# Optimization experiments

Measured on AMD Instinct MI355X. Metric: run time of the kernel, lower is better.

Reference implementation:

```python
import jax, jax.numpy as jnp
import numpy as np

N = 100000      # total nodes (flattened batch)
E = 640000      # total edges
D = 128         # in_channels
SIM_THR = 0.2   # pt_dict['sim_pt']
DEG_THR = 3.0   # pt_dict['degree_pt']
PT_THRESHOLD = 0.1  # edge-pruning cosine threshold
EPS = 1e-8      # F.cosine_similarity eps


def _glorot(key, shape):
    a = np.sqrt(6.0 / (shape[-2] + shape[-1]))
    return jax.random.uniform(key, shape, jnp.float32, -a, a)


def setup_inputs() -> dict:
    key = jax.random.key(0)
    k1, k2, k3, k4, k5 = jax.random.split(key, 5)
    x = jax.random.normal(k1, (N, D), jnp.float32)
    edge_index = jax.random.randint(k2, (2, E), 0, N, dtype=jnp.int32)
    p_sim = _glorot(k3, (1, D))
    p_deg = _glorot(k4, (1, D))
    p_other = _glorot(k5, (1, D))
    return {"x": x, "edge_index": edge_index, "p_sim": p_sim, "p_deg": p_deg, "p_other": p_other}


def reference(x, edge_index, p_sim, p_deg, p_other):
    n = x.shape[0]
    row, col = edge_index[0], edge_index[1]

    # --- sim_pt: per-edge cosine of raw features, scatter-add to dst, degree-normalize ---
    x_norm = x / jnp.sqrt(jnp.sum(x * x, axis=1, keepdims=True))          # [N, D]
    e = jnp.sum(x_norm[row] * x_norm[col], axis=1)                         # [E]
    c = jax.ops.segment_sum(e, col, num_segments=n)                        # [N]
    deg = jax.ops.segment_sum(jnp.ones_like(e), col, num_segments=n)       # [N]
    # torch: c/deg -> nan for deg==0, nan <= thr is False; +inf gives the same mask, safely.
    csim = jnp.where(deg > 0, c / jnp.maximum(deg, 1.0), jnp.inf)
    mask_sim = csim <= SIM_THR                                             # [N]

    # --- degree_pt ---
    mask_deg = deg <= DEG_THR                                              # [N]

    # --- other_pt == 'all': nodes that got no prompt so far ---
    mask_other = ~(mask_sim | mask_deg)                                    # [N]

    # g_mutiftpt_record: [N, 3, D], slot filled with its prompt row where mask else 0
    masks = jnp.stack([mask_sim, mask_deg, mask_other], axis=1)            # [N, 3]
    prompts = jnp.concatenate([p_sim, p_deg, p_other], axis=0)             # [3, D]
    record = masks[:, :, None].astype(x.dtype) * prompts[None, :, :]       # [N, 3, D]

    # use_attention=False branch: mean over non-padding (all-nonzero) slots
    wo_pad = jnp.all(record != 0, axis=-1)                                 # [N, 3]
    plen = jnp.sum(wo_pad, axis=1, keepdims=True).astype(x.dtype)          # [N, 1]
    final = jnp.where(plen > 0, record.sum(axis=1) / jnp.maximum(plen, 1.0), 0.0)  # [N, D]

    x_new = x + final                                                      # add_pt

    # edge pruning by cosine similarity of prompted features (F.cosine_similarity, eps=1e-8)
    nrm = jnp.sqrt(jnp.sum(x_new * x_new, axis=1))                         # [N]
    na = jnp.maximum(nrm[row], EPS)
    nb = jnp.maximum(nrm[col], EPS)
    cos = jnp.sum(x_new[row] * x_new[col], axis=1) / (na * nb)             # [E]
    keep_edges = cos >= PT_THRESHOLD                                       # [E] bool mask (edge list is static-shape; mask instead of compaction)
    return x_new, keep_edges
```

## Files before the change

### kernel.cpp

```cpp
#include <hip/hip_runtime.h>
#include <hip/hip_bf16.h>
#include <math.h>

#define D_DIM 128
#define SIM_THR 0.2f
#define DEG_THR 3.0f
#define PT_THR 0.1
#define EPS_CS 1e-8
#define MARGIN 4e-3f
#define PK 4294967296.0

typedef unsigned short u16;

#define WS_NEED 8960064

__device__ __forceinline__ float bf2f(u16 u) {
    return __uint_as_float(((unsigned)u) << 16);
}

__global__ void prompt_pre_kernel(const float* __restrict__ ps,
                                  const float* __restrict__ pd,
                                  const float* __restrict__ po,
                                  int* __restrict__ flags,
                                  float* __restrict__ G) {
    int t = threadIdx.x;
    float s0 = ps[t], s1 = ps[t + 64];
    float d0 = pd[t], d1 = pd[t + 64];
    float o0 = po[t], o1 = po[t + 64];
    float ss = s0 * s0 + s1 * s1;
    float sd = s0 * d0 + s1 * d1;
    float so = s0 * o0 + s1 * o1;
    float dd = d0 * d0 + d1 * d1;
    float dO = d0 * o0 + d1 * o1;
    float oo = o0 * o0 + o1 * o1;
    for (int m = 32; m; m >>= 1) {
        ss += __shfl_xor(ss, m);
        sd += __shfl_xor(sd, m);
        so += __shfl_xor(so, m);
        dd += __shfl_xor(dd, m);
        dO += __shfl_xor(dO, m);
        oo += __shfl_xor(oo, m);
    }
    unsigned long long zs = __ballot(s0 == 0.0f || s1 == 0.0f);
    unsigned long long zd = __ballot(d0 == 0.0f || d1 == 0.0f);
    unsigned long long zo = __ballot(o0 == 0.0f || o1 == 0.0f);
    if (t == 0) {
        flags[0] = (zs == 0ull);
        flags[1] = (zd == 0ull);
        flags[2] = (zo == 0ull);
        G[0] = ss; G[1] = sd; G[2] = so;
        G[3] = sd; G[4] = dd; G[5] = dO;
        G[6] = so; G[7] = dO; G[8] = oo;
    }
}

__global__ void node_pre_kernel(const float* __restrict__ x,
                                const float* __restrict__ ps,
                                const float* __restrict__ pd,
                                const float* __restrict__ po,
                                u16* __restrict__ xnorm,
                                float* __restrict__ nx,
                                float* __restrict__ rs,
                                float* __restrict__ rd,
                                float* __restrict__ ro, int N) {
    int g = threadIdx.x >> 5;
    int lane = threadIdx.x & 31;
    int n = blockIdx.x * 8 + g;
    if (n >= N) return;
    int off = lane * 4;
    const float4 v = *(const float4*)(x + (size_t)n * D_DIM + off);
    const float4 s = *(const float4*)(ps + off);
    const float4 d = *(const float4*)(pd + off);
    const float4 o = *(const float4*)(po + off);
    float sq = v.x * v.x + v.y * v.y + v.z * v.z + v.w * v.w;
    float drs = v.x * s.x + v.y * s.y + v.z * s.z + v.w * s.w;
    float drd = v.x * d.x + v.y * d.y + v.z * d.z + v.w * d.w;
    float dro = v.x * o.x + v.y * o.y + v.z * o.z + v.w * o.w;
    for (int m = 16; m; m >>= 1) {
        sq += __shfl_xor(sq, m, 32);
        drs += __shfl_xor(drs, m, 32);
        drd += __shfl_xor(drd, m, 32);
        dro += __shfl_xor(dro, m, 32);
    }
    float nrm = sqrtf(sq);
    float inv = 1.0f / nrm;
    __hip_bfloat16 ob[4];
    ob[0] = __float2bfloat16(v.x * inv);
    ob[1] = __float2bfloat16(v.y * inv);
    ob[2] = __float2bfloat16(v.z * inv);
    ob[3] = __float2bfloat16(v.w * inv);
    *(ushort4*)(xnorm + (size_t)n * D_DIM + off) =
        make_ushort4(*(u16*)&ob[0], *(u16*)&ob[1], *(u16*)&ob[2], *(u16*)&ob[3]);
    if (lane == 0) {
        nx[n] = nrm;
        rs[n] = drs;
        rd[n] = drd;
        ro[n] = dro;
    }
}

__global__ void edge_sim_kernel(const u16* __restrict__ xnorm,
                                const int* __restrict__ ei,
                                double* __restrict__ cd,
                                float* __restrict__ e_arr,
                                int E) {
    int lane = threadIdx.x & 31;
    int grp = blockIdx.x * 8 + (threadIdx.x >> 5);
    int base = grp * 4;
    if (base >= E) return;

    int r[4], c4[4];
    #pragma unroll
    for (int k = 0; k < 4; ++k) {
        int e = base + k;
        int src = (e < E) ? e : base;
        r[k] = ei[src];
        c4[k] = ei[E + src];
    }

    ushort4 a[4], b[4];
    #pragma unroll
    for (int k = 0; k < 4; ++k) {
        a[k] = *(const ushort4*)(xnorm + (size_t)r[k] * D_DIM + lane * 4);
        b[k] = *(const ushort4*)(xnorm + (size_t)c4[k] * D_DIM + lane * 4);
    }

    float d[4];
    #pragma unroll
    for (int k = 0; k < 4; ++k) {
        d[k] = bf2f(a[k].x) * bf2f(b[k].x) + bf2f(a[k].y) * bf2f(b[k].y) +
               bf2f(a[k].z) * bf2f(b[k].z) + bf2f(a[k].w) * bf2f(b[k].w);
    }
    for (int m = 16; m; m >>= 1) {
        #pragma unroll
        for (int k = 0; k < 4; ++k) d[k] += __shfl_xor(d[k], m, 32);
    }

    if (lane < 4) {
        int e = base + lane;
        if (e < E) {
            float dv = (lane == 0) ? d[0] : (lane == 1) ? d[1] : (lane == 2) ? d[2] : d[3];
            if (e_arr) e_arr[e] = dv;
            atomicAdd(&cd[c4[lane]], (double)dv + PK);
        }
    }
}

__global__ void node_prompt_kernel(const float* __restrict__ x,
                                   const double* __restrict__ cd,
                                   const float* __restrict__ ps,
                                   const float* __restrict__ pd,
                                   const float* __restrict__ po,
                                   const int* __restrict__ flags,
                                   const float* __restrict__ nx,
                                   const float* __restrict__ rs,
                                   const float* __restrict__ rd,
                                   const float* __restrict__ ro,
                                   float* __restrict__ xn,
                                   double* __restrict__ na,
                                   float* __restrict__ pack, int N) {
    int g = threadIdx.x >> 5;
    int lane = threadIdx.x & 31;
    int n = blockIdx.x * 8 + g;
    if (n >= N) return;
    double v = cd[n];
    double degd = floor(v * (1.0 / PK) + 0.5);
    float dg = (float)degd;
    float cc = (float)(v - degd * PK);
    float csim = (dg > 0.0f) ? (cc / fmaxf(dg, 1.0f)) : INFINITY;
    bool ms = (csim <= SIM_THR);
    bool md = (dg <= DEG_THR);
    bool mo = !(ms || md);
    int plen = (ms && flags[0]) + (md && flags[1]) + (mo && flags[2]);
    float invp = (plen > 0) ? (1.0f / (float)plen) : 0.0f;

    int off = lane * 4;
    const float4 xv = *(const float4*)(x + (size_t)n * D_DIM + off);
    const float4 s  = *(const float4*)(ps + off);
    const float4 dd = *(const float4*)(pd + off);
    const float4 o  = *(const float4*)(po + off);

    float4 f;
    f.x = (ms ? s.x : 0.0f) + (md ? dd.x : 0.0f) + (mo ? o.x : 0.0f);
    f.y = (ms ? s.y : 0.0f) + (md ? dd.y : 0.0f) + (mo ? o.y : 0.0f);
    f.z = (ms ? s.z : 0.0f) + (md ? dd.z : 0.0f) + (mo ? o.z : 0.0f);
    f.w = (ms ? s.w : 0.0f) + (md ? dd.w : 0.0f) + (mo ? o.w : 0.0f);

    float4 r;
    r.x = xv.x + f.x * invp;
    r.y = xv.y + f.y * invp;
    r.z = xv.z + f.z * invp;
    r.w = xv.w + f.w * invp;

    *(float4*)(xn + (size_t)n * D_DIM + off) = r;

    double sq = (double)r.x * r.x + (double)r.y * r.y + (double)r.z * r.z + (double)r.w * r.w;
    for (int m = 16; m; m >>= 1) sq += __shfl_xor(sq, m, 32);
    if (lane == 0) {
        double nrm = sqrt(sq);
        double nad = (nrm > EPS_CS) ? nrm : EPS_CS;
        na[n] = nad;
        if (pack) {
            float as = ms ? invp : 0.0f;
            float ad = md ? invp : 0.0f;
            float ao = mo ? invp : 0.0f;
            float4 w0 = make_float4(rs[n], rd[n], ro[n], nx[n]);
            float4 w1 = make_float4(as, ad, ao, (float)(1.0 / nad));
            *(float4*)(pack + (size_t)n * 8)     = w0;
            *(float4*)(pack + (size_t)n * 8 + 4) = w1;
        }
    }
}

__global__ void edge_prune_fused(const int* __restrict__ ei,
                                 const float* __restrict__ e_arr,
                                 const float* __restrict__ pack,
                                 const float* __restrict__ G,
                                 const float* __restrict__ xn,
                                 const double* __restrict__ na,
                                 float* __restrict__ keep, int E) {
    __shared__ int s_list[256];
    __shared__ int s_cnt;
    int tid = threadIdx.x;
    if (tid == 0) s_cnt = 0;
    __syncthreads();

    int e = blockIdx.x * 256 + tid;
    if (e < E) {
        int i = ei[e], j = ei[E + e];
        const float4 ri = *(const float4*)(pack + (size_t)i * 8);
        const float4 ai = *(const float4*)(pack + (size_t)i * 8 + 4);
        const float4 rj = *(const float4*)(pack + (size_t)j * 8);
        const float4 aj = *(const float4*)(pack + (size_t)j * 8 + 4);
        float ev = e_arr[e];
        float dot = ev * ri.w * rj.w
                  + aj.x * ri.x + aj.y * ri.y + aj.z * ri.z
                  + ai.x * rj.x + ai.y * rj.y + ai.z * rj.z;
        dot += ai.x * (G[0] * aj.x + G[1] * aj.y + G[2] * aj.z)
             + ai.y * (G[3] * aj.x + G[4] * aj.y + G[5] * aj.z)
             + ai.z * (G[6] * aj.x + G[7] * aj.y + G[8] * aj.z);
        float cosv = dot * ai.w * aj.w;
        keep[e] = (cosv >= 0.1f) ? 1.0f : 0.0f;
        if (fabsf(cosv - 0.1f) < MARGIN) {
            int idx = atomicAdd(&s_cnt, 1);
            s_list[idx] = e;
        }
    }
    __syncthreads();

    int cnt = s_cnt;
    int lane = tid & 31;
    int grp = tid >> 5;
    for (int it = grp; it < cnt; it += 8) {
        int ee = s_list[it];
        int row = ei[ee], col = ei[E + ee];
        const float4 a = *(const float4*)(xn + (size_t)row * D_DIM + lane * 4);
        const float4 b = *(const float4*)(xn + (size_t)col * D_DIM + lane * 4);
        double d = (double)a.x * b.x + (double)a.y * b.y +
                   (double)a.z * b.z + (double)a.w * b.w;
        for (int m = 16; m; m >>= 1) d += __shfl_xor(d, m, 32);
        if (lane == 0) {
            double cs = d / (na[row] * na[col]);
            keep[ee] = (cs >= PT_THR) ? 1.0f : 0.0f;
        }
    }
}

__global__ void edge_prune_kernel(const float* __restrict__ xn,
                                  const int* __restrict__ ei,
                                  const double* __restrict__ na,
                                  float* __restrict__ keep, int E) {
    int lane = threadIdx.x & 31;
    int grp = blockIdx.x * 8 + (threadIdx.x >> 5);
    int e0 = grp * 2, e1 = e0 + 1;
    if (e0 >= E) return;
    bool has1 = (e1 < E);
    int row0 = ei[e0], col0 = ei[E + e0];
    int row1 = has1 ? ei[e1] : row0;
    int col1 = has1 ? ei[E + e1] : col0;

    const float4 a0 = *(const float4*)(xn + (size_t)row0 * D_DIM + lane * 4);
    const float4 b0 = *(const float4*)(xn + (size_t)col0 * D_DIM + lane * 4);
    const float4 a1 = *(const float4*)(xn + (size_t)row1 * D_DIM + lane * 4);
    const float4 b1 = *(const float4*)(xn + (size_t)col1 * D_DIM + lane * 4);

    double d0 = (double)a0.x * b0.x + (double)a0.y * b0.y +
                (double)a0.z * b0.z + (double)a0.w * b0.w;
    double d1 = (double)a1.x * b1.x + (double)a1.y * b1.y +
                (double)a1.z * b1.z + (double)a1.w * b1.w;
    for (int m = 16; m; m >>= 1) {
        d0 += __shfl_xor(d0, m, 32);
        d1 += __shfl_xor(d1, m, 32);
    }
    if (lane == 0) {
        double cs = d0 / (na[row0] * na[col0]);
        keep[e0] = (cs >= PT_THR) ? 1.0f : 0.0f;
    } else if (lane == 1 && has1) {
        double cs = d1 / (na[row1] * na[col1]);
        keep[e1] = (cs >= PT_THR) ? 1.0f : 0.0f;
    }
}

extern "C" void kernel_launch(void* const* d_in, const int* in_sizes, int n_in,
                              void* d_out, int out_size, void* d_ws, size_t ws_size,
                              hipStream_t stream) {
    const float* x  = (const float*)d_in[0];
    const int*   ei = (const int*)d_in[1];
    const float* ps = (const float*)d_in[2];
    const float* pd = (const float*)d_in[3];
    const float* po = (const float*)d_in[4];

    const int N = in_sizes[0] / D_DIM;
    const int E = in_sizes[1] / 2;

    float* xn    = (float*)d_out;
    float* keep  = (float*)d_out + (size_t)N * D_DIM;
    u16*   xnorm = (u16*)d_out;

    char* ws = (char*)d_ws;
    const int nodeBlocks = (N + 7) / 8;
    const int simBlocks  = (E + 31) / 32;

    if (ws_size >= (size_t)WS_NEED) {
        double* cd    = (double*)(ws + 0);
        double* na    = (double*)(ws + 800000);
        float* nx     = (float*)(ws + 1600000);
        float* rs     = (float*)(ws + 2000000);
        float* rd     = (float*)(ws + 2400000);
        float* ro     = (float*)(ws + 2800000);
        float* e_arr  = (float*)(ws + 3200000);
        float* pack   = (float*)(ws + 5760000);
        int*   flags  = (int*)(ws + 8960000);
        float* G      = (float*)(ws + 8960016);

        hipMemsetAsync(cd, 0, 800000, stream);

        prompt_pre_kernel<<<1, 64, 0, stream>>>(ps, pd, po, flags, G);
        node_pre_kernel<<<nodeBlocks, 256, 0, stream>>>(x, ps, pd, po, xnorm, nx, rs, rd, ro, N);
        edge_sim_kernel<<<simBlocks, 256, 0, stream>>>(xnorm, ei, cd, e_arr, E);
        node_prompt_kernel<<<nodeBlocks, 256, 0, stream>>>(x, cd, ps, pd, po,
                                                           flags, nx, rs, rd, ro,
                                                           xn, na, pack, N);
        edge_prune_fused<<<(E + 255) / 256, 256, 0, stream>>>(ei, e_arr, pack, G, xn, na, keep, E);
    } else {
        double* cd    = (double*)(ws + 0);
        double* na    = (double*)(ws + 800000);
        int*   flags  = (int*)(ws + 1600000);
        float* G      = (float*)(ws + 1600016);
        float* scratch = (float*)(ws + 1600064);

        hipMemsetAsync(cd, 0, 800000, stream);
        prompt_pre_kernel<<<1, 64, 0, stream>>>(ps, pd, po, flags, G);
        node_pre_kernel<<<nodeBlocks, 256, 0, stream>>>(x, ps, pd, po, xnorm,
                                                        scratch, scratch, scratch, scratch, N);
        edge_sim_kernel<<<simBlocks, 256, 0, stream>>>(xnorm, ei, cd, nullptr, E);
        node_prompt_kernel<<<nodeBlocks, 256, 0, stream>>>(x, cd, ps, pd, po,
                                                           flags, nullptr, nullptr, nullptr, nullptr,
                                                           xn, na, nullptr, N);
        edge_prune_kernel<<<(E + 15) / 16, 256, 0, stream>>>(xn, ei, na, keep, E);
    }
}
```

Before: 107.6 us.

## Partition edge-sim atomics by destination range per XCD and fuse prep kernels

The edge similarity kernel now has each block take a chunk of edges and filter, into shared memory, only those whose destination node falls in the range assigned to that block's XCD (blockIdx mod 8). The aim is to keep the double-precision scatter atomics for a node range inside one XCD's L2. The memset of the accumulator and the prompt precompute kernel are folded into node_pre_kernel, removing two launches. In exchange, every block rereads the column indices for its chunk (8x redundant index reads), compacts the list with a shared atomic counter, and relies on blocks being assigned to XCDs round-robin.

```diff
diff --git a/kernel.cpp b/kernel.cpp
--- a/kernel.cpp
+++ b/kernel.cpp
@@ -9,6 +9,8 @@
 #define EPS_CS 1e-8
 #define MARGIN 4e-3f
 #define PK 4294967296.0
+#define CHUNK 2048
+#define NXCD 8
 
 typedef unsigned short u16;
 
@@ -16,42 +18,6 @@
 
 __device__ __forceinline__ float bf2f(u16 u) {
     return __uint_as_float(((unsigned)u) << 16);
-}
-
-__global__ void prompt_pre_kernel(const float* __restrict__ ps,
-                                  const float* __restrict__ pd,
-                                  const float* __restrict__ po,
-                                  int* __restrict__ flags,
-                                  float* __restrict__ G) {
-    int t = threadIdx.x;
-    float s0 = ps[t], s1 = ps[t + 64];
-    float d0 = pd[t], d1 = pd[t + 64];
-    float o0 = po[t], o1 = po[t + 64];
-    float ss = s0 * s0 + s1 * s1;
-    float sd = s0 * d0 + s1 * d1;
-    float so = s0 * o0 + s1 * o1;
-    float dd = d0 * d0 + d1 * d1;
-    float dO = d0 * o0 + d1 * o1;
-    float oo = o0 * o0 + o1 * o1;
-    for (int m = 32; m; m >>= 1) {
-        ss += __shfl_xor(ss, m);
-        sd += __shfl_xor(sd, m);
-        so += __shfl_xor(so, m);
-        dd += __shfl_xor(dd, m);
-        dO += __shfl_xor(dO, m);
-        oo += __shfl_xor(oo, m);
-    }
-    unsigned long long zs = __ballot(s0 == 0.0f || s1 == 0.0f);
-    unsigned long long zd = __ballot(d0 == 0.0f || d1 == 0.0f);
-    unsigned long long zo = __ballot(o0 == 0.0f || o1 == 0.0f);
-    if (t == 0) {
-        flags[0] = (zs == 0ull);
-        flags[1] = (zd == 0ull);
-        flags[2] = (zo == 0ull);
-        G[0] = ss; G[1] = sd; G[2] = so;
-        G[3] = sd; G[4] = dd; G[5] = dO;
-        G[6] = so; G[7] = dO; G[8] = oo;
-    }
 }
 
 __global__ void node_pre_kernel(const float* __restrict__ x,
@@ -62,86 +28,146 @@
                                 float* __restrict__ nx,
                                 float* __restrict__ rs,
                                 float* __restrict__ rd,
-                                float* __restrict__ ro, int N) {
+                                float* __restrict__ ro,
+                                double* __restrict__ cd,
+                                int* __restrict__ flags,
+                                float* __restrict__ G, int N) {
     int g = threadIdx.x >> 5;
     int lane = threadIdx.x & 31;
     int n = blockIdx.x * 8 + g;
-    if (n >= N) return;
-    int off = lane * 4;
-    const float4 v = *(const float4*)(x + (size_t)n * D_DIM + off);
-    const float4 s = *(const float4*)(ps + off);
-    const float4 d = *(const float4*)(pd + off);
-    const float4 o = *(const float4*)(po + off);
-    float sq = v.x * v.x + v.y * v.y + v.z * v.z + v.w * v.w;
-    float drs = v.x * s.x + v.y * s.y + v.z * s.z + v.w * s.w;
-    float drd = v.x * d.x + v.y * d.y + v.z * d.z + v.w * d.w;
-    float dro = v.x * o.x + v.y * o.y + v.z * o.z + v.w * o.w;
-    for (int m = 16; m; m >>= 1) {
-        sq += __shfl_xor(sq, m, 32);
-        drs += __shfl_xor(drs, m, 32);
-        drd += __shfl_xor(drd, m, 32);
-        dro += __shfl_xor(dro, m, 32);
-    }
-    float nrm = sqrtf(sq);
-    float inv = 1.0f / nrm;
-    __hip_bfloat16 ob[4];
-    ob[0] = __float2bfloat16(v.x * inv);
-    ob[1] = __float2bfloat16(v.y * inv);
-    ob[2] = __float2bfloat16(v.z * inv);
-    ob[3] = __float2bfloat16(v.w * inv);
-    *(ushort4*)(xnorm + (size_t)n * D_DIM + off) =
-        make_ushort4(*(u16*)&ob[0], *(u16*)&ob[1], *(u16*)&ob[2], *(u16*)&ob[3]);
-    if (lane == 0) {
-        nx[n] = nrm;
-        rs[n] = drs;
-        rd[n] = drd;
-        ro[n] = dro;
-    }
-}
-
-__global__ void edge_sim_kernel(const u16* __restrict__ xnorm,
-                                const int* __restrict__ ei,
-                                double* __restrict__ cd,
-                                float* __restrict__ e_arr,
-                                int E) {
-    int lane = threadIdx.x & 31;
-    int grp = blockIdx.x * 8 + (threadIdx.x >> 5);
-    int base = grp * 4;
-    if (base >= E) return;
-
-    int r[4], c4[4];
-    #pragma unroll
-    for (int k = 0; k < 4; ++k) {
-        int e = base + k;
-        int src = (e < E) ? e : base;
-        r[k] = ei[src];
-        c4[k] = ei[E + src];
-    }
-
-    ushort4 a[4], b[4];
-    #pragma unroll
-    for (int k = 0; k < 4; ++k) {
-        a[k] = *(const ushort4*)(xnorm + (size_t)r[k] * D_DIM + lane * 4);
-        b[k] = *(const ushort4*)(xnorm + (size_t)c4[k] * D_DIM + lane * 4);
-    }
-
-    float d[4];
-    #pragma unroll
-    for (int k = 0; k < 4; ++k) {
-        d[k] = bf2f(a[k].x) * bf2f(b[k].x) + bf2f(a[k].y) * bf2f(b[k].y) +
-               bf2f(a[k].z) * bf2f(b[k].z) + bf2f(a[k].w) * bf2f(b[k].w);
-    }
-    for (int m = 16; m; m >>= 1) {
+    if (n < N) {
+        int off = lane * 4;
+        const float4 v = *(const float4*)(x + (size_t)n * D_DIM + off);
+        const float4 s = *(const float4*)(ps + off);
+        const float4 d = *(const float4*)(pd + off);
+        const float4 o = *(const float4*)(po + off);
+        float sq = v.x * v.x + v.y * v.y + v.z * v.z + v.w * v.w;
+        float drs = v.x * s.x + v.y * s.y + v.z * s.z + v.w * s.w;
+        float drd = v.x * d.x + v.y * d.y + v.z * d.z + v.w * d.w;
+        float dro = v.x * o.x + v.y * o.y + v.z * o.z + v.w * o.w;
+        for (int m = 16; m; m >>= 1) {
+            sq += __shfl_xor(sq, m, 32);
+            drs += __shfl_xor(drs, m, 32);
+            drd += __shfl_xor(drd, m, 32);
+            dro += __shfl_xor(dro, m, 32);
+        }
+        float nrm = sqrtf(sq);
+        float inv = 1.0f / nrm;
+        __hip_bfloat16 ob[4];
+        ob[0] = __float2bfloat16(v.x * inv);
+        ob[1] = __float2bfloat16(v.y * inv);
+        ob[2] = __float2bfloat16(v.z * inv);
+        ob[3] = __float2bfloat16(v.w * inv);
+        *(ushort4*)(xnorm + (size_t)n * D_DIM + off) =
+            make_ushort4(*(u16*)&ob[0], *(u16*)&ob[1], *(u16*)&ob[2], *(u16*)&ob[3]);
+        if (lane == 0) {
+            nx[n] = nrm;
+            rs[n] = drs;
+            rd[n] = drd;
+            ro[n] = dro;
+            cd[n] = 0.0;
+        }
+    }
+    if (blockIdx.x == 0 && threadIdx.x < 64) {
+        int t = threadIdx.x;
+        float s0 = ps[t], s1 = ps[t + 64];
+        float d0 = pd[t], d1 = pd[t + 64];
+        float o0 = po[t], o1 = po[t + 64];
+        float ss = s0 * s0 + s1 * s1;
+        float sd = s0 * d0 + s1 * d1;
+        float so = s0 * o0 + s1 * o1;
+        float dd = d0 * d0 + d1 * d1;
+        float dO = d0 * o0 + d1 * o1;
+        float oo = o0 * o0 + o1 * o1;
+        for (int m = 32; m; m >>= 1) {
+            ss += __shfl_xor(ss, m);
+            sd += __shfl_xor(sd, m);
+            so += __shfl_xor(so, m);
+            dd += __shfl_xor(dd, m);
+            dO += __shfl_xor(dO, m);
+            oo += __shfl_xor(oo, m);
+        }
+        unsigned long long zs = __ballot(s0 == 0.0f || s1 == 0.0f);
+        unsigned long long zd = __ballot(d0 == 0.0f || d1 == 0.0f);
+        unsigned long long zo = __ballot(o0 == 0.0f || o1 == 0.0f);
+        if (t == 0) {
+            flags[0] = (zs == 0ull);
+            flags[1] = (zd == 0ull);
+            flags[2] = (zo == 0ull);
+            G[0] = ss; G[1] = sd; G[2] = so;
+            G[3] = sd; G[4] = dd; G[5] = dO;
+            G[6] = so; G[7] = dO; G[8] = oo;
+        }
+    }
+}
+
+__global__ void edge_sim_part(const u16* __restrict__ xnorm,
+                              const int* __restrict__ ei,
+                              double* __restrict__ cd,
+                              float* __restrict__ e_arr,
+                              int E, int N) {
+    __shared__ int s_list[CHUNK];
+    __shared__ int s_cnt;
+    int tid = threadIdx.x;
+    if (tid == 0) s_cnt = 0;
+    __syncthreads();
+
+    int xcd = blockIdx.x & (NXCD - 1);
+    int base = (blockIdx.x >> 3) * CHUNK;
+    int range = (N + NXCD - 1) / NXCD;
+    int lo = xcd * range;
+    int hi = min(N, lo + range);
+
+    for (int i = tid; i < CHUNK; i += 256) {
+        int e = base + i;
+        if (e < E) {
+            int col = ei[E + e];
+            if (col >= lo && col < hi) {
+                int idx = atomicAdd(&s_cnt, 1);
+                s_list[idx] = e;
+            }
+        }
+    }
+    __syncthreads();
+
+    int cnt = s_cnt;
+    int lane = tid & 31;
+    int grp = tid >> 5;
+    for (int b = grp * 4; b < cnt; b += 32) {
+        int r[4], c4[4];
         #pragma unroll
-        for (int k = 0; k < 4; ++k) d[k] += __shfl_xor(d[k], m, 32);
-    }
-
-    if (lane < 4) {
-        int e = base + lane;
-        if (e < E) {
-            float dv = (lane == 0) ? d[0] : (lane == 1) ? d[1] : (lane == 2) ? d[2] : d[3];
-            if (e_arr) e_arr[e] = dv;
-            atomicAdd(&cd[c4[lane]], (double)dv + PK);
+        for (int k = 0; k < 4; ++k) {
+            int p = b + k;
+            int src = s_list[(p < cnt) ? p : b];
+            r[k] = ei[src];
+            c4[k] = ei[E + src];
+        }
+        ushort4 a[4], bb[4];
+        #pragma unroll
+        for (int k = 0; k < 4; ++k) {
+            a[k]  = *(const ushort4*)(xnorm + (size_t)r[k] * D_DIM + lane * 4);
+            bb[k] = *(const ushort4*)(xnorm + (size_t)c4[k] * D_DIM + lane * 4);
+        }
+        float d[4];
+        #pragma unroll
+        for (int k = 0; k < 4; ++k) {
+            d[k] = bf2f(a[k].x) * bf2f(bb[k].x) + bf2f(a[k].y) * bf2f(bb[k].y) +
+                   bf2f(a[k].z) * bf2f(bb[k].z) + bf2f(a[k].w) * bf2f(bb[k].w);
+        }
+        for (int m = 16; m; m >>= 1) {
+            #pragma unroll
+            for (int k = 0; k < 4; ++k) d[k] += __shfl_xor(d[k], m, 32);
+        }
+        if (lane < 4) {
+            int p = b + lane;
+            if (p < cnt) {
+                int e = s_list[p];
+                int col = ei[E + e];
+                float dv = (lane == 0) ? d[0] : (lane == 1) ? d[1]
+                         : (lane == 2) ? d[2] : d[3];
+                if (e_arr) e_arr[e] = dv;
+                atomicAdd(&cd[col], (double)dv + PK);
+            }
         }
     }
 }
@@ -319,7 +345,7 @@
 
     char* ws = (char*)d_ws;
     const int nodeBlocks = (N + 7) / 8;
-    const int simBlocks  = (E + 31) / 32;
+    const int simBlocks  = ((E + CHUNK - 1) / CHUNK) * NXCD;
 
     if (ws_size >= (size_t)WS_NEED) {
         double* cd    = (double*)(ws + 0);
@@ -333,11 +359,9 @@
         int*   flags  = (int*)(ws + 8960000);
         float* G      = (float*)(ws + 8960016);
 
-        hipMemsetAsync(cd, 0, 800000, stream);
-
-        prompt_pre_kernel<<<1, 64, 0, stream>>>(ps, pd, po, flags, G);
-        node_pre_kernel<<<nodeBlocks, 256, 0, stream>>>(x, ps, pd, po, xnorm, nx, rs, rd, ro, N);
-        edge_sim_kernel<<<simBlocks, 256, 0, stream>>>(xnorm, ei, cd, e_arr, E);
+        node_pre_kernel<<<nodeBlocks, 256, 0, stream>>>(x, ps, pd, po, xnorm,
+                                                        nx, rs, rd, ro, cd, flags, G, N);
+        edge_sim_part<<<simBlocks, 256, 0, stream>>>(xnorm, ei, cd, e_arr, E, N);
         node_prompt_kernel<<<nodeBlocks, 256, 0, stream>>>(x, cd, ps, pd, po,
                                                            flags, nx, rs, rd, ro,
                                                            xn, na, pack, N);
@@ -349,11 +373,10 @@
         float* G      = (float*)(ws + 1600016);
         float* scratch = (float*)(ws + 1600064);
 
-        hipMemsetAsync(cd, 0, 800000, stream);
-        prompt_pre_kernel<<<1, 64, 0, stream>>>(ps, pd, po, flags, G);
         node_pre_kernel<<<nodeBlocks, 256, 0, stream>>>(x, ps, pd, po, xnorm,
-                                                        scratch, scratch, scratch, scratch, N);
-        edge_sim_kernel<<<simBlocks, 256, 0, stream>>>(xnorm, ei, cd, nullptr, E);
+                                                        scratch, scratch, scratch, scratch,
+                                                        cd, flags, G, N);
+        edge_sim_part<<<simBlocks, 256, 0, stream>>>(xnorm, ei, cd, nullptr, E, N);
         node_prompt_kernel<<<nodeBlocks, 256, 0, stream>>>(x, cd, ps, pd, po,
                                                            flags, nullptr, nullptr, nullptr, nullptr,
                                                            xn, na, nullptr, N);
```

New measurement: 115.8 us. 1.08x slower.

## Fold memset and prompt precompute into node_pre; widen edge_sim to 8 edges per group

Applied to the files above, without the earlier changes.

Removes the separate hipMemsetAsync of the per-node accumulator and the one-block prompt_pre launch. The zeroing moves into node_pre_kernel, written per node, and block 0 computes the prompt Gram matrix and flags. The edge similarity kernel now processes 8 edges per 32-lane group instead of 4, halving the grid and doubling gathers in flight per thread. The cost is more registers per thread in edge_sim, and the early return in node_pre is replaced by a guarded branch so block 0 can still run the prompt code.

```diff
diff --git a/kernel.cpp b/kernel.cpp
--- a/kernel.cpp
+++ b/kernel.cpp
@@ -16,42 +16,6 @@
 
 __device__ __forceinline__ float bf2f(u16 u) {
     return __uint_as_float(((unsigned)u) << 16);
-}
-
-__global__ void prompt_pre_kernel(const float* __restrict__ ps,
-                                  const float* __restrict__ pd,
-                                  const float* __restrict__ po,
-                                  int* __restrict__ flags,
-                                  float* __restrict__ G) {
-    int t = threadIdx.x;
-    float s0 = ps[t], s1 = ps[t + 64];
-    float d0 = pd[t], d1 = pd[t + 64];
-    float o0 = po[t], o1 = po[t + 64];
-    float ss = s0 * s0 + s1 * s1;
-    float sd = s0 * d0 + s1 * d1;
-    float so = s0 * o0 + s1 * o1;
-    float dd = d0 * d0 + d1 * d1;
-    float dO = d0 * o0 + d1 * o1;
-    float oo = o0 * o0 + o1 * o1;
-    for (int m = 32; m; m >>= 1) {
-        ss += __shfl_xor(ss, m);
-        sd += __shfl_xor(sd, m);
-        so += __shfl_xor(so, m);
-        dd += __shfl_xor(dd, m);
-        dO += __shfl_xor(dO, m);
-        oo += __shfl_xor(oo, m);
-    }
-    unsigned long long zs = __ballot(s0 == 0.0f || s1 == 0.0f);
-    unsigned long long zd = __ballot(d0 == 0.0f || d1 == 0.0f);
-    unsigned long long zo = __ballot(o0 == 0.0f || o1 == 0.0f);
-    if (t == 0) {
-        flags[0] = (zs == 0ull);
-        flags[1] = (zd == 0ull);
-        flags[2] = (zo == 0ull);
-        G[0] = ss; G[1] = sd; G[2] = so;
-        G[3] = sd; G[4] = dd; G[5] = dO;
-        G[6] = so; G[7] = dO; G[8] = oo;
-    }
 }
 
 __global__ void node_pre_kernel(const float* __restrict__ x,
@@ -62,40 +26,76 @@
                                 float* __restrict__ nx,
                                 float* __restrict__ rs,
                                 float* __restrict__ rd,
-                                float* __restrict__ ro, int N) {
+                                float* __restrict__ ro,
+                                double* __restrict__ cd,
+                                int* __restrict__ flags,
+                                float* __restrict__ G, int N) {
     int g = threadIdx.x >> 5;
     int lane = threadIdx.x & 31;
     int n = blockIdx.x * 8 + g;
-    if (n >= N) return;
-    int off = lane * 4;
-    const float4 v = *(const float4*)(x + (size_t)n * D_DIM + off);
-    const float4 s = *(const float4*)(ps + off);
-    const float4 d = *(const float4*)(pd + off);
-    const float4 o = *(const float4*)(po + off);
-    float sq = v.x * v.x + v.y * v.y + v.z * v.z + v.w * v.w;
-    float drs = v.x * s.x + v.y * s.y + v.z * s.z + v.w * s.w;
-    float drd = v.x * d.x + v.y * d.y + v.z * d.z + v.w * d.w;
-    float dro = v.x * o.x + v.y * o.y + v.z * o.z + v.w * o.w;
-    for (int m = 16; m; m >>= 1) {
-        sq += __shfl_xor(sq, m, 32);
-        drs += __shfl_xor(drs, m, 32);
-        drd += __shfl_xor(drd, m, 32);
-        dro += __shfl_xor(dro, m, 32);
-    }
-    float nrm = sqrtf(sq);
-    float inv = 1.0f / nrm;
-    __hip_bfloat16 ob[4];
-    ob[0] = __float2bfloat16(v.x * inv);
-    ob[1] = __float2bfloat16(v.y * inv);
-    ob[2] = __float2bfloat16(v.z * inv);
-    ob[3] = __float2bfloat16(v.w * inv);
-    *(ushort4*)(xnorm + (size_t)n * D_DIM + off) =
-        make_ushort4(*(u16*)&ob[0], *(u16*)&ob[1], *(u16*)&ob[2], *(u16*)&ob[3]);
-    if (lane == 0) {
-        nx[n] = nrm;
-        rs[n] = drs;
-        rd[n] = drd;
-        ro[n] = dro;
+    if (n < N) {
+        int off = lane * 4;
+        const float4 v = *(const float4*)(x + (size_t)n * D_DIM + off);
+        const float4 s = *(const float4*)(ps + off);
+        const float4 d = *(const float4*)(pd + off);
+        const float4 o = *(const float4*)(po + off);
+        float sq = v.x * v.x + v.y * v.y + v.z * v.z + v.w * v.w;
+        float drs = v.x * s.x + v.y * s.y + v.z * s.z + v.w * s.w;
+        float drd = v.x * d.x + v.y * d.y + v.z * d.z + v.w * d.w;
+        float dro = v.x * o.x + v.y * o.y + v.z * o.z + v.w * o.w;
+        for (int m = 16; m; m >>= 1) {
+            sq += __shfl_xor(sq, m, 32);
+            drs += __shfl_xor(drs, m, 32);
+            drd += __shfl_xor(drd, m, 32);
+            dro += __shfl_xor(dro, m, 32);
+        }
+        float nrm = sqrtf(sq);
+        float inv = 1.0f / nrm;
+        __hip_bfloat16 ob[4];
+        ob[0] = __float2bfloat16(v.x * inv);
+        ob[1] = __float2bfloat16(v.y * inv);
+        ob[2] = __float2bfloat16(v.z * inv);
+        ob[3] = __float2bfloat16(v.w * inv);
+        *(ushort4*)(xnorm + (size_t)n * D_DIM + off) =
+            make_ushort4(*(u16*)&ob[0], *(u16*)&ob[1], *(u16*)&ob[2], *(u16*)&ob[3]);
+        if (lane == 0) {
+            nx[n] = nrm;
+            rs[n] = drs;
+            rd[n] = drd;
+            ro[n] = dro;
+            cd[n] = 0.0;
+        }
+    }
+    if (blockIdx.x == 0 && threadIdx.x < 64) {
+        int t = threadIdx.x;
+        float s0 = ps[t], s1 = ps[t + 64];
+        float d0 = pd[t], d1 = pd[t + 64];
+        float o0 = po[t], o1 = po[t + 64];
+        float ss = s0 * s0 + s1 * s1;
+        float sd = s0 * d0 + s1 * d1;
+        float so = s0 * o0 + s1 * o1;
+        float dd = d0 * d0 + d1 * d1;
+        float dO = d0 * o0 + d1 * o1;
+        float oo = o0 * o0 + o1 * o1;
+        for (int m = 32; m; m >>= 1) {
+            ss += __shfl_xor(ss, m);
+            sd += __shfl_xor(sd, m);
+            so += __shfl_xor(so, m);
+            dd += __shfl_xor(dd, m);
+            dO += __shfl_xor(dO, m);
+            oo += __shfl_xor(oo, m);
+        }
+        unsigned long long zs = __ballot(s0 == 0.0f || s1 == 0.0f);
+        unsigned long long zd = __ballot(d0 == 0.0f || d1 == 0.0f);
+        unsigned long long zo = __ballot(o0 == 0.0f || o1 == 0.0f);
+        if (t == 0) {
+            flags[0] = (zs == 0ull);
+            flags[1] = (zd == 0ull);
+            flags[2] = (zo == 0ull);
+            G[0] = ss; G[1] = sd; G[2] = so;
+            G[3] = sd; G[4] = dd; G[5] = dO;
+            G[6] = so; G[7] = dO; G[8] = oo;
+        }
     }
 }
 
@@ -106,42 +106,49 @@
                                 int E) {
     int lane = threadIdx.x & 31;
     int grp = blockIdx.x * 8 + (threadIdx.x >> 5);
-    int base = grp * 4;
+    int base = grp * 8;
     if (base >= E) return;
 
-    int r[4], c4[4];
+    int r[8], c8[8];
     #pragma unroll
-    for (int k = 0; k < 4; ++k) {
+    for (int k = 0; k < 8; ++k) {
         int e = base + k;
         int src = (e < E) ? e : base;
         r[k] = ei[src];
-        c4[k] = ei[E + src];
-    }
-
-    ushort4 a[4], b[4];
+        c8[k] = ei[E + src];
+    }
+
+    ushort4 a[8], b[8];
     #pragma unroll
-    for (int k = 0; k < 4; ++k) {
+    for (int k = 0; k < 8; ++k) {
         a[k] = *(const ushort4*)(xnorm + (size_t)r[k] * D_DIM + lane * 4);
-        b[k] = *(const ushort4*)(xnorm + (size_t)c4[k] * D_DIM + lane * 4);
-    }
-
-    float d[4];
+        b[k] = *(const ushort4*)(xnorm + (size_t)c8[k] * D_DIM + lane * 4);
+    }
+
+    float d[8];
     #pragma unroll
-    for (int k = 0; k < 4; ++k) {
+    for (int k = 0; k < 8; ++k) {
         d[k] = bf2f(a[k].x) * bf2f(b[k].x) + bf2f(a[k].y) * bf2f(b[k].y) +
                bf2f(a[k].z) * bf2f(b[k].z) + bf2f(a[k].w) * bf2f(b[k].w);
     }
     for (int m = 16; m; m >>= 1) {
         #pragma unroll
-        for (int k = 0; k < 4; ++k) d[k] += __shfl_xor(d[k], m, 32);
-    }
-
-    if (lane < 4) {
+        for (int k = 0; k < 8; ++k) d[k] += __shfl_xor(d[k], m, 32);
+    }
+
+    if (lane < 8) {
         int e = base + lane;
         if (e < E) {
-            float dv = (lane == 0) ? d[0] : (lane == 1) ? d[1] : (lane == 2) ? d[2] : d[3];
+            float dv = (lane == 0) ? d[0] : (lane == 1) ? d[1]
+                     : (lane == 2) ? d[2] : (lane == 3) ? d[3]
+                     : (lane == 4) ? d[4] : (lane == 5) ? d[5]
+                     : (lane == 6) ? d[6] : d[7];
+            int cc = (lane == 0) ? c8[0] : (lane == 1) ? c8[1]
+                   : (lane == 2) ? c8[2] : (lane == 3) ? c8[3]
+                   : (lane == 4) ? c8[4] : (lane == 5) ? c8[5]
+                   : (lane == 6) ? c8[6] : c8[7];
             if (e_arr) e_arr[e] = dv;
-            atomicAdd(&cd[c4[lane]], (double)dv + PK);
+            atomicAdd(&cd[cc], (double)dv + PK);
         }
     }
 }
@@ -319,7 +326,7 @@
 
     char* ws = (char*)d_ws;
     const int nodeBlocks = (N + 7) / 8;
-    const int simBlocks  = (E + 31) / 32;
+    const int simBlocks  = (E + 63) / 64;
 
     if (ws_size >= (size_t)WS_NEED) {
         double* cd    = (double*)(ws + 0);
@@ -333,10 +340,8 @@
         int*   flags  = (int*)(ws + 8960000);
         float* G      = (float*)(ws + 8960016);
 
-        hipMemsetAsync(cd, 0, 800000, stream);
-
-        prompt_pre_kernel<<<1, 64, 0, stream>>>(ps, pd, po, flags, G);
-        node_pre_kernel<<<nodeBlocks, 256, 0, stream>>>(x, ps, pd, po, xnorm, nx, rs, rd, ro, N);
+        node_pre_kernel<<<nodeBlocks, 256, 0, stream>>>(x, ps, pd, po, xnorm,
+                                                        nx, rs, rd, ro, cd, flags, G, N);
         edge_sim_kernel<<<simBlocks, 256, 0, stream>>>(xnorm, ei, cd, e_arr, E);
         node_prompt_kernel<<<nodeBlocks, 256, 0, stream>>>(x, cd, ps, pd, po,
                                                            flags, nx, rs, rd, ro,
@@ -349,10 +354,9 @@
         float* G      = (float*)(ws + 1600016);
         float* scratch = (float*)(ws + 1600064);
 
-        hipMemsetAsync(cd, 0, 800000, stream);
-        prompt_pre_kernel<<<1, 64, 0, stream>>>(ps, pd, po, flags, G);
         node_pre_kernel<<<nodeBlocks, 256, 0, stream>>>(x, ps, pd, po, xnorm,
-                                                        scratch, scratch, scratch, scratch, N);
+                                                        scratch, scratch, scratch, scratch,
+                                                        cd, flags, G, N);
         edge_sim_kernel<<<simBlocks, 256, 0, stream>>>(xnorm, ei, cd, nullptr, E);
         node_prompt_kernel<<<nodeBlocks, 256, 0, stream>>>(x, cd, ps, pd, po,
                                                            flags, nullptr, nullptr, nullptr, nullptr,
```

Result: faster. 101.2 us (-6.0%).
